# Optimization experiments

Hardware: AMD Instinct MI355X
Metric: run time of the kernel (lower is better)

## Reference

```python
import jax, jax.numpy as jnp
import numpy as np

D_MODEL = 1024
NUM_HEADS = 16
D_K = D_MODEL // NUM_HEADS
B, S = 4, 2048


def setup_inputs() -> dict:
    key = jax.random.key(0)
    ks = jax.random.split(key, 12)
    scale = 1.0 / np.sqrt(D_MODEL)
    inp = {
        "q": jax.random.normal(ks[0], (B, S, D_MODEL), dtype=jnp.float32),
        "k": jax.random.normal(ks[1], (B, S, D_MODEL), dtype=jnp.float32),
        "v": jax.random.normal(ks[2], (B, S, D_MODEL), dtype=jnp.float32),
        "mask": jnp.ones((B, 1, 1, S), dtype=jnp.int32),
        "Wq": jax.random.normal(ks[3], (D_MODEL, D_MODEL), dtype=jnp.float32) * scale,
        "bq": jnp.zeros((D_MODEL,), dtype=jnp.float32),
        "Wk": jax.random.normal(ks[4], (D_MODEL, D_MODEL), dtype=jnp.float32) * scale,
        "bk": jnp.zeros((D_MODEL,), dtype=jnp.float32),
        "Wv": jax.random.normal(ks[5], (D_MODEL, D_MODEL), dtype=jnp.float32) * scale,
        "bv": jnp.zeros((D_MODEL,), dtype=jnp.float32),
        "Wo": jax.random.normal(ks[6], (D_MODEL, D_MODEL), dtype=jnp.float32) * scale,
        "bo": jnp.zeros((D_MODEL,), dtype=jnp.float32),
    }
    return inp


def reference(q, k, v, mask, Wq, bq, Wk, bk, Wv, bv, Wo, bo):
    b, s, d = q.shape
    # QKV projections (torch Linear: x @ W.T + b; here weights stored as (d,d) used as x @ W + b)
    query = (q @ Wq + bq).reshape(b, s, NUM_HEADS, D_K).transpose(0, 2, 1, 3)  # (b,h,s,dk)
    key_ = (k @ Wk + bk).reshape(b, s, NUM_HEADS, D_K).transpose(0, 2, 1, 3)
    value = (v @ Wv + bv).reshape(b, s, NUM_HEADS, D_K).transpose(0, 2, 1, 3)
    # full score matrix (b,h,s,s), scaled by sqrt(d_k)
    scores = jnp.einsum("bhqd,bhkd->bhqk", query, key_) / jnp.sqrt(jnp.float32(D_K))
    scores = jnp.where(mask == 0, jnp.float32(-jnp.inf), scores)
    attn = jax.nn.softmax(scores, axis=-1)
    # dropout p=0.0 (eval) -> identity
    out = jnp.einsum("bhqk,bhkd->bhqd", attn, value)  # (b,h,s,dk)
    out = out.transpose(0, 2, 1, 3).reshape(b, s, NUM_HEADS * D_K)
    return out @ Wo + bo
```

## Files before the change

### kernel.cpp

```cpp
#include <hip/hip_runtime.h>

typedef __attribute__((ext_vector_type(8)))  short  short8;
typedef __attribute__((ext_vector_type(4)))  short  short4v;
typedef __attribute__((ext_vector_type(4)))  float  f32x4;
typedef __attribute__((ext_vector_type(16))) float  f32x16;
typedef __attribute__((ext_vector_type(8)))  __bf16 bf8_t;
typedef __attribute__((ext_vector_type(4)))  __bf16 bf4_t;
typedef __attribute__((ext_vector_type(2)))  __bf16 bf2_t;
typedef __attribute__((ext_vector_type(4)))  unsigned uint4v;

#define DMODEL 1024
#define SEQ    2048
#define NB     4
#define NH     16
#define MTOT   (NB * SEQ)
#define DM2    ((size_t)DMODEL * DMODEL)
#define SCALE_LOG2E 0.18033688011112042f
#define CSTRIDE 512
#define TSPAN   (8 * CSTRIDE)

static __device__ __forceinline__ ushort f2bf(float f) {
  union { float f; unsigned u; } v; v.f = f;
  unsigned r = v.u + 0x7fffu + ((v.u >> 16) & 1u);
  return (ushort)(r >> 16);
}

static __device__ __forceinline__ float fexp2(float x) {
#if __has_builtin(__builtin_amdgcn_exp2f)
  return __builtin_amdgcn_exp2f(x);
#else
  return __expf(x * 0.6931471805599453f);
#endif
}

static __device__ __forceinline__ f32x4 mfma32(short8 a, short8 b, f32x4 c) {
  return __builtin_amdgcn_mfma_f32_16x16x32_bf16(
      __builtin_bit_cast(bf8_t, a), __builtin_bit_cast(bf8_t, b), c, 0, 0, 0);
}

static __device__ __forceinline__ f32x16 mfma3232(short8 a, short8 b, f32x16 c) {
  return __builtin_amdgcn_mfma_f32_32x32x16_bf16(
      __builtin_bit_cast(bf8_t, a), __builtin_bit_cast(bf8_t, b), c, 0, 0, 0);
}

static __device__ __forceinline__ unsigned pk2(float a, float b) {
  bf2_t t; t[0] = (__bf16)a; t[1] = (__bf16)b;
  return __builtin_bit_cast(unsigned, t);
}

static __device__ __forceinline__ void plswap(unsigned& a, unsigned& b) {
  asm volatile("v_permlane32_swap_b32 %0, %1" : "+v"(a), "+v"(b));
}

static __device__ __forceinline__ void gl_lds16(const ushort* g, ushort* l) {
  __builtin_amdgcn_global_load_lds(
      (const __attribute__((address_space(1))) unsigned*)(unsigned long long)g,
      (__attribute__((address_space(3))) unsigned*)(unsigned long long)l,
      16, 0, 0);
}

__global__ __launch_bounds__(256) void cvt3_k(
    const float* __restrict__ q, const float* __restrict__ k,
    const float* __restrict__ v, ushort* __restrict__ qb,
    ushort* __restrict__ kb, ushort* __restrict__ vb,
    const int* __restrict__ mask, float* __restrict__ biasf,
    unsigned* __restrict__ flags) {
  const int z = blockIdx.y;
  if (z == 0 && blockIdx.x < 32) {
    const int t = blockIdx.x * 256 + threadIdx.x;
    const int m = mask[t];
    biasf[t] = m ? 0.f : -1e30f;
    const unsigned long long bal = __ballot(m == 0);
    if ((threadIdx.x & 63) == 0)
      flags[blockIdx.x * 4 + (threadIdx.x >> 6)] = (bal != 0ull) ? 1u : 0u;
  }
  const float* src = (z == 0) ? q : (z == 1) ? k : v;
  ushort* dst = (z == 0) ? qb : (z == 1) ? kb : vb;
  const size_t i = ((size_t)blockIdx.x * 256 + threadIdx.x) * 8;
  const float4 a0 = *(const float4*)&src[i];
  const float4 a1 = *(const float4*)&src[i + 4];
  bf8_t c;
  c[0] = (__bf16)a0.x; c[1] = (__bf16)a0.y; c[2] = (__bf16)a0.z; c[3] = (__bf16)a0.w;
  c[4] = (__bf16)a1.x; c[5] = (__bf16)a1.y; c[6] = (__bf16)a1.z; c[7] = (__bf16)a1.w;
  *(short8*)&dst[i] = __builtin_bit_cast(short8, c);
}

__global__ __launch_bounds__(1024) void wtrans_k(
    const float* __restrict__ Wq, const float* __restrict__ Wk,
    const float* __restrict__ Wv, const float* __restrict__ Wo,
    ushort* __restrict__ Wt) {
  __shared__ float tile[32][33];
  const int z = blockIdx.z;
  const float* W = (z == 0) ? Wq : (z == 1) ? Wk : (z == 2) ? Wv : Wo;
  ushort* out = Wt + (size_t)z * DM2;
  const int tx = threadIdx.x, ty = threadIdx.y;
  const int n0 = blockIdx.x * 32, k0 = blockIdx.y * 32;
  tile[ty][tx] = W[(size_t)(k0 + ty) * DMODEL + n0 + tx];
  __syncthreads();
  out[(size_t)(n0 + ty) * DMODEL + k0 + tx] = f2bf(tile[tx][ty]);
}

#define GEMM_BODY(A, Bt, M0v, N0v)                                              \
  __shared__ ushort Asm[128 * 64];                                              \
  __shared__ ushort Bsm[128 * 64];                                              \
  const int tid = threadIdx.x;                                                  \
  const int wid = tid >> 6, lane = tid & 63;                                    \
  const int wr = wid >> 1, wc = wid & 1;                                        \
  const int lr = lane & 15, lg = lane >> 4;                                     \
  const int m0 = (M0v), n0 = (N0v);                                             \
  const int sr8 = lane >> 3, sg = ((lane & 7) ^ sr8) * 8;                       \
  size_t gA[4], gB[4];                                                          \
  ushort *lA[4], *lB[4];                                                        \
  _Pragma("unroll") for (int j = 0; j < 4; j++) {                               \
    const int ch = wid * 4 + j;                                                 \
    gA[j] = (size_t)(m0 + ch * 8 + sr8) * DMODEL + sg;                          \
    gB[j] = (size_t)(n0 + ch * 8 + sr8) * DMODEL + sg;                          \
    lA[j] = &Asm[ch * 512];                                                     \
    lB[j] = &Bsm[ch * 512];                                                     \
  }                                                                             \
  f32x4 acc[4][4];                                                              \
  _Pragma("unroll") for (int m = 0; m < 4; m++)                                 \
      _Pragma("unroll") for (int n = 0; n < 4; n++)                             \
          acc[m][n] = (f32x4){0.f, 0.f, 0.f, 0.f};                              \
  _Pragma("unroll") for (int j = 0; j < 4; j++) {                               \
    gl_lds16(&A[gA[j]], lA[j]);                                                 \
    gl_lds16(&Bt[gB[j]], lB[j]);                                                \
  }                                                                             \
  const int soff = (lg ^ (lr & 7)) * 8;                                         \
  for (int ks = 0; ks < DMODEL / 64; ++ks) {                                    \
    __syncthreads();                                                            \
    _Pragma("unroll") for (int kk = 0; kk < 2; kk++) {                          \
      const int sx = soff ^ (kk * 32);                                          \
      short8 af[4], bfr[4];                                                     \
      _Pragma("unroll") for (int m = 0; m < 4; m++) af[m] =                     \
          *(const short8*)&Asm[(wr * 64 + m * 16 + lr) * 64 + sx];              \
      _Pragma("unroll") for (int n = 0; n < 4; n++) bfr[n] =                    \
          *(const short8*)&Bsm[(wc * 64 + n * 16 + lr) * 64 + sx];              \
      _Pragma("unroll") for (int m = 0; m < 4; m++)                             \
          _Pragma("unroll") for (int n = 0; n < 4; n++)                         \
              acc[m][n] = mfma32(af[m], bfr[n], acc[m][n]);                     \
    }                                                                           \
    __syncthreads();                                                            \
    if (ks < DMODEL / 64 - 1) {                                                 \
      const size_t ko = (size_t)(ks + 1) * 64;                                  \
      _Pragma("unroll") for (int j = 0; j < 4; j++) {                           \
        gl_lds16(&A[gA[j] + ko], lA[j]);                                        \
        gl_lds16(&Bt[gB[j] + ko], lB[j]);                                       \
      }                                                                         \
    }                                                                           \
  }

__global__ __launch_bounds__(256) void gemmqkv_k(
    const ushort* __restrict__ qb, const ushort* __restrict__ kb,
    const ushort* __restrict__ vb, const ushort* __restrict__ Wt,
    const float* __restrict__ bq, const float* __restrict__ bk,
    const float* __restrict__ bv, ushort* __restrict__ Qp,
    ushort* __restrict__ Kp, ushort* __restrict__ Vb) {
  const int z = blockIdx.z;
  const int bx = blockIdx.x, by = blockIdx.y;
  const ushort* A  = (z == 0) ? Wt : (z == 1) ? (Wt + DM2) : vb;
  const ushort* Bm = (z == 0) ? qb : (z == 1) ? kb : (Wt + 2 * DM2);
  const int M0 = (z == 2) ? bx * 128 : by * 128;
  const int N0 = (z == 2) ? by * 128 : bx * 128;
  GEMM_BODY(A, Bm, M0, N0)

  if (z == 2) {
    float bv4[4];
#pragma unroll
    for (int n = 0; n < 4; n++) bv4[n] = bv[n0 + wc * 64 + n * 16 + lr];
#pragma unroll
    for (int m = 0; m < 4; m++) {
      const int grb = m0 + wr * 64 + m * 16 + lg * 4;
#pragma unroll
      for (int n = 0; n < 4; n++) {
        const int gc = n0 + wc * 64 + n * 16 + lr;
        const int hh = gc >> 6, dk = gc & 63;
        const int bb = grb >> 11, ss = grb & 2047;
        bf4_t pk;
#pragma unroll
        for (int j = 0; j < 4; j++) pk[j] = (__bf16)(acc[m][n][j] + bv4[n]);
        const int swz = ((dk & 7) * 8) ^ (((dk >> 3) & 3) * 16);
        const size_t addr = (((size_t)bb * NH + hh) * SEQ) * 64 +
                            (size_t)(ss >> 6) * 4096 + dk * 64 +
                            ((ss & 63) ^ swz);
        *(short4v*)&Vb[addr] = __builtin_bit_cast(short4v, pk);
      }
    }
  } else {
    const float* bias = (z == 0) ? bq : bk;
    ushort* out = (z == 0) ? Qp : Kp;
    const float scale = (z == 0) ? SCALE_LOG2E : 1.f;
#pragma unroll
    for (int m = 0; m < 4; m++) {
      const int f0 = m0 + wr * 64 + m * 16 + lg * 4;
      const f32x4 b4 = *(const f32x4*)&bias[f0];
      const int hh = f0 >> 6, dk0 = f0 & 63;
#pragma unroll
      for (int n = 0; n < 4; n++) {
        const int t = n0 + wc * 64 + n * 16 + lr;
        const int b = t >> 11, s = t & 2047;
        bf4_t pk;
#pragma unroll
        for (int j = 0; j < 4; j++)
          pk[j] = (__bf16)((acc[m][n][j] + b4[j]) * scale);
        size_t addr;
        if (z == 0) {
          addr = (((size_t)b * NH + hh) * SEQ + s) * 64 + dk0;
        } else {
          const int swz = ((s & 7) * 8) ^ (((s >> 3) & 3) * 16);
          addr = (((size_t)b * NH + hh) * SEQ) * 64 + (size_t)(s >> 6) * 4096 +
                 (s & 63) * 64 + (dk0 ^ swz);
        }
        *(short4v*)&out[addr] = __builtin_bit_cast(short4v, pk);
      }
    }
  }
}

__global__ __launch_bounds__(256) void gemmo_k(
    const ushort* __restrict__ Ain, const ushort* __restrict__ Btin,
    const float* __restrict__ bias, float* __restrict__ out) {
  GEMM_BODY(Ain, Btin, blockIdx.x * 128, blockIdx.y * 128)
  float bv4[4];
#pragma unroll
  for (int n = 0; n < 4; n++) bv4[n] = bias[n0 + wc * 64 + n * 16 + lr];
#pragma unroll
  for (int m = 0; m < 4; m++) {
    const int grb = m0 + wr * 64 + m * 16 + lg * 4;
#pragma unroll
    for (int n = 0; n < 4; n++) {
      const int gc = n0 + wc * 64 + n * 16 + lr;
#pragma unroll
      for (int j = 0; j < 4; j++)
        out[(size_t)(grb + j) * DMODEL + gc] = acc[m][n][j] + bv4[n];
    }
  }
}

__global__ __launch_bounds__(256) void attn_k(
    const ushort* __restrict__ Qp, const ushort* __restrict__ Kp,
    const ushort* __restrict__ Vt, const float* __restrict__ biasf,
    const unsigned* __restrict__ flags, ushort* __restrict__ ctx) {
  __shared__ ushort smem[4 * TSPAN];
  const int tid = threadIdx.x, w = tid >> 6, lane = tid & 63;
  const int q = lane & 31, hi = lane >> 5;
  const int n = blockIdx.x;
  const int xcd = n & 7, idx = n >> 3;
  const int bh = ((idx >> 4) << 3) | xcd;
  const int qt = idx & 15;
  const int b = bh >> 4, h = bh & 15;
  const int q0w = qt * 128 + w * 32;
  const ushort* Qh = Qp + (size_t)bh * SEQ * 64;
  const ushort* Kh = Kp + (size_t)bh * SEQ * 64;
  const ushort* Vh = Vt + (size_t)bh * SEQ * 64;
  const float* biasb = biasf + b * SEQ;
  const unsigned* flb = flags + b * 32;

  short8 qf[4];
#pragma unroll
  for (int c = 0; c < 4; c++)
    qf[c] = *(const short8*)&Qh[(size_t)(q0w + q) * 64 + c * 16 + hi * 8];

  const int xo = ((q & 7) * 8) ^ (((q >> 3) & 3) * 16);
  const int rbase = q * 64;
  int off[4];
#pragma unroll
  for (int c = 0; c < 4; c++) off[c] = rbase + ((c * 16 + hi * 8) ^ xo);

  const int sl = lane * 8;
  const int c0 = 2 * w, c1 = 2 * w + 1;

  f32x16 o0, o1;
#pragma unroll
  for (int r = 0; r < 16; r++) { o0[r] = 0.f; o1[r] = 0.f; }
  float l_run = 0.f;

  gl_lds16(&Kh[c0 * 512 + sl], &smem[c0 * CSTRIDE]);
  gl_lds16(&Kh[c1 * 512 + sl], &smem[c1 * CSTRIDE]);
  gl_lds16(&Vh[c0 * 512 + sl], &smem[2 * TSPAN + c0 * CSTRIDE]);
  gl_lds16(&Vh[c1 * 512 + sl], &smem[2 * TSPAN + c1 * CSTRIDE]);
  __syncthreads();

  for (int it = 0; it < 32; ++it) {
    const int cur = it & 1;
    if (it < 31) {
      const size_t tb = (size_t)(it + 1) * 4096;
      ushort* kd = &smem[(cur ^ 1) * TSPAN];
      ushort* vd = &smem[2 * TSPAN + (cur ^ 1) * TSPAN];
      gl_lds16(&Kh[tb + c0 * 512 + sl], &kd[c0 * CSTRIDE]);
      gl_lds16(&Kh[tb + c1 * 512 + sl], &kd[c1 * CSTRIDE]);
      gl_lds16(&Vh[tb + c0 * 512 + sl], &vd[c0 * CSTRIDE]);
      gl_lds16(&Vh[tb + c1 * 512 + sl], &vd[c1 * CSTRIDE]);
    }

    const ushort* kl = &smem[cur * TSPAN];
    const ushort* vl = &smem[2 * TSPAN + cur * TSPAN];

    f32x16 s0, s1;
#pragma unroll
    for (int r = 0; r < 16; r++) { s0[r] = 0.f; s1[r] = 0.f; }
#pragma unroll
    for (int c = 0; c < 4; c++)
      s0 = mfma3232(*(const short8*)&kl[off[c]], qf[c], s0);
#pragma unroll
    for (int c = 0; c < 4; c++)
      s1 = mfma3232(*(const short8*)&kl[off[c] + 2048], qf[c], s1);

    float p[32];
    if (flb[it]) {
      const float* bp = biasb + it * 64;
#pragma unroll
      for (int kt = 0; kt < 2; kt++)
#pragma unroll
        for (int g = 0; g < 4; g++) {
          const f32x4 ba = *(const f32x4*)&bp[kt * 32 + g * 8 + hi * 4];
#pragma unroll
          for (int j = 0; j < 4; j++)
            p[kt * 16 + g * 4 + j] =
                fexp2((kt ? s1[g * 4 + j] : s0[g * 4 + j]) + ba[j]);
        }
    } else {
#pragma unroll
      for (int r = 0; r < 16; r++) {
        p[r] = fexp2(s0[r]);
        p[16 + r] = fexp2(s1[r]);
      }
    }

    float a16[16], a8[8], a4[4];
#pragma unroll
    for (int i = 0; i < 16; i++) a16[i] = p[i] + p[16 + i];
#pragma unroll
    for (int i = 0; i < 8; i++) a8[i] = a16[i] + a16[8 + i];
#pragma unroll
    for (int i = 0; i < 4; i++) a4[i] = a8[i] + a8[4 + i];
    float ps = (a4[0] + a4[1]) + (a4[2] + a4[3]);
    ps += __shfl_xor(ps, 32);
    l_run += ps;

    short8 frag[4];
#pragma unroll
    for (int kb = 0; kb < 4; kb++) {
      unsigned X0 = pk2(p[8 * kb + 0], p[8 * kb + 1]);
      unsigned X1 = pk2(p[8 * kb + 2], p[8 * kb + 3]);
      unsigned Y0 = pk2(p[8 * kb + 4], p[8 * kb + 5]);
      unsigned Y1 = pk2(p[8 * kb + 6], p[8 * kb + 7]);
      plswap(X0, Y0);
      plswap(X1, Y1);
      frag[kb] = __builtin_bit_cast(short8, (uint4v){X0, X1, Y0, Y1});
    }

#pragma unroll
    for (int kb = 0; kb < 4; kb++) {
      o0 = mfma3232(*(const short8*)&vl[off[kb]], frag[kb], o0);
      o1 = mfma3232(*(const short8*)&vl[off[kb] + 2048], frag[kb], o1);
    }

    __syncthreads();
  }

  const float inv = 1.f / l_run;
  ushort* ow = &smem[w * 2176];
#pragma unroll
  for (int r = 0; r < 16; r++) {
    const int dk = (r & 3) + 8 * (r >> 2) + 4 * hi;
    ow[q * 68 + dk] = __builtin_bit_cast(ushort, (__bf16)(o0[r] * inv));
    ow[q * 68 + 32 + dk] = __builtin_bit_cast(ushort, (__bf16)(o1[r] * inv));
  }
  __syncthreads();
  const int sr = lane >> 4, dc = (lane & 15) * 4;
#pragma unroll
  for (int i = 0; i < 8; i++) {
    const int qq = i * 4 + sr;
    const short4v vv = *(const short4v*)&ow[qq * 68 + dc];
    *(short4v*)&ctx[((size_t)b * SEQ + q0w + qq) * DMODEL + h * 64 + dc] = vv;
  }
}

extern "C" void kernel_launch(void* const* d_in, const int* in_sizes, int n_in,
                              void* d_out, int out_size, void* d_ws,
                              size_t ws_size, hipStream_t stream) {
  const float* q    = (const float*)d_in[0];
  const float* k    = (const float*)d_in[1];
  const float* v    = (const float*)d_in[2];
  const int*   mask = (const int*)d_in[3];
  const float* Wq   = (const float*)d_in[4];
  const float* bq   = (const float*)d_in[5];
  const float* Wk   = (const float*)d_in[6];
  const float* bk   = (const float*)d_in[7];
  const float* Wv   = (const float*)d_in[8];
  const float* bv   = (const float*)d_in[9];
  const float* Wo   = (const float*)d_in[10];
  const float* bo   = (const float*)d_in[11];

  char* p = (char*)d_ws;
  ushort* Wt = (ushort*)p; p += (size_t)4 * DM2 * 2;
  ushort* Qp = (ushort*)p; p += (size_t)MTOT * DMODEL * 2;
  ushort* Kp = (ushort*)p; p += (size_t)MTOT * DMODEL * 2;
  ushort* Vb = (ushort*)p; p += (size_t)MTOT * DMODEL * 2;
  ushort* qb = (ushort*)p; p += (size_t)MTOT * DMODEL * 2;
  ushort* kb = (ushort*)p; p += (size_t)MTOT * DMODEL * 2;
  ushort* vb = (ushort*)p; p += (size_t)MTOT * DMODEL * 2;
  float*  biasf = (float*)p; p += (size_t)NB * SEQ * 4;
  unsigned* flags = (unsigned*)p;
  ushort* ctx = qb;

  wtrans_k<<<dim3(32, 32, 4), dim3(32, 32), 0, stream>>>(Wq, Wk, Wv, Wo, Wt);
  cvt3_k<<<dim3(MTOT * DMODEL / (256 * 8), 3), 256, 0, stream>>>(
      q, k, v, qb, kb, vb, mask, biasf, flags);

  gemmqkv_k<<<dim3(MTOT / 128, DMODEL / 128, 3), 256, 0, stream>>>(
      qb, kb, vb, Wt, bq, bk, bv, Qp, Kp, Vb);

  attn_k<<<1024, 256, 0, stream>>>(Qp, Kp, Vb, biasf, flags, ctx);

  gemmo_k<<<dim3(MTOT / 128, DMODEL / 128), 256, 0, stream>>>(
      ctx, Wt + (size_t)3 * DM2, bo, (float*)d_out);
}
```

Before: 208.2 us.

## Double-buffer GEMM LDS tiles with half-depth K steps and one barrier

Rewrites the shared GEMM body to use two LDS buffers of 128x32 bf16 tiles instead of one 128x64 tile. The next K slice is prefetched into the alternate buffer while MFMAs run on the current one, so each iteration needs one barrier instead of two. The aim is to hide global-to-LDS load latency behind compute. In exchange there are twice as many loop iterations with a smaller K step. The XOR swizzle is narrowed to four 16-byte chunks per row, which may raise LDS bank conflicts.

```diff
diff --git a/kernel.cpp b/kernel.cpp
--- a/kernel.cpp
+++ b/kernel.cpp
@@ -100,54 +100,55 @@
   out[(size_t)(n0 + ty) * DMODEL + k0 + tx] = f2bf(tile[tx][ty]);
 }
 
-#define GEMM_BODY(A, Bt, M0v, N0v)                                              \
-  __shared__ ushort Asm[128 * 64];                                              \
-  __shared__ ushort Bsm[128 * 64];                                              \
-  const int tid = threadIdx.x;                                                  \
-  const int wid = tid >> 6, lane = tid & 63;                                    \
-  const int wr = wid >> 1, wc = wid & 1;                                        \
-  const int lr = lane & 15, lg = lane >> 4;                                     \
-  const int m0 = (M0v), n0 = (N0v);                                             \
-  const int sr8 = lane >> 3, sg = ((lane & 7) ^ sr8) * 8;                       \
-  size_t gA[4], gB[4];                                                          \
-  ushort *lA[4], *lB[4];                                                        \
-  _Pragma("unroll") for (int j = 0; j < 4; j++) {                               \
-    const int ch = wid * 4 + j;                                                 \
-    gA[j] = (size_t)(m0 + ch * 8 + sr8) * DMODEL + sg;                          \
-    gB[j] = (size_t)(n0 + ch * 8 + sr8) * DMODEL + sg;                          \
-    lA[j] = &Asm[ch * 512];                                                     \
-    lB[j] = &Bsm[ch * 512];                                                     \
-  }                                                                             \
-  f32x4 acc[4][4];                                                              \
-  _Pragma("unroll") for (int m = 0; m < 4; m++)                                 \
-      _Pragma("unroll") for (int n = 0; n < 4; n++)                             \
-          acc[m][n] = (f32x4){0.f, 0.f, 0.f, 0.f};                              \
-  _Pragma("unroll") for (int j = 0; j < 4; j++) {                               \
-    gl_lds16(&A[gA[j]], lA[j]);                                                 \
-    gl_lds16(&Bt[gB[j]], lB[j]);                                                \
-  }                                                                             \
-  const int soff = (lg ^ (lr & 7)) * 8;                                         \
-  for (int ks = 0; ks < DMODEL / 64; ++ks) {                                    \
-    __syncthreads();                                                            \
-    _Pragma("unroll") for (int kk = 0; kk < 2; kk++) {                          \
-      const int sx = soff ^ (kk * 32);                                          \
-      short8 af[4], bfr[4];                                                     \
-      _Pragma("unroll") for (int m = 0; m < 4; m++) af[m] =                     \
-          *(const short8*)&Asm[(wr * 64 + m * 16 + lr) * 64 + sx];              \
-      _Pragma("unroll") for (int n = 0; n < 4; n++) bfr[n] =                    \
-          *(const short8*)&Bsm[(wc * 64 + n * 16 + lr) * 64 + sx];              \
-      _Pragma("unroll") for (int m = 0; m < 4; m++)                             \
-          _Pragma("unroll") for (int n = 0; n < 4; n++)                         \
-              acc[m][n] = mfma32(af[m], bfr[n], acc[m][n]);                     \
-    }                                                                           \
-    __syncthreads();                                                            \
-    if (ks < DMODEL / 64 - 1) {                                                 \
-      const size_t ko = (size_t)(ks + 1) * 64;                                  \
-      _Pragma("unroll") for (int j = 0; j < 4; j++) {                           \
-        gl_lds16(&A[gA[j] + ko], lA[j]);                                        \
-        gl_lds16(&Bt[gB[j] + ko], lB[j]);                                       \
-      }                                                                         \
-    }                                                                           \
+#define GEMM_BODY(A, Bt, M0v, N0v)                                             \
+  __shared__ ushort Asm[2][128 * 32];                                          \
+  __shared__ ushort Bsm[2][128 * 32];                                          \
+  const int tid = threadIdx.x;                                                 \
+  const int wid = tid >> 6, lane = tid & 63;                                   \
+  const int wr = wid >> 1, wc = wid & 1;                                       \
+  const int lr = lane & 15, lg = lane >> 4;                                    \
+  const int m0 = (M0v), n0 = (N0v);                                            \
+  const int srow = lane >> 2;                                                  \
+  const int sgr = ((lane & 3) ^ (srow & 3)) * 8;                               \
+  size_t gA[2], gB[2];                                                         \
+  int lco[2];                                                                  \
+  _Pragma("unroll") for (int j = 0; j < 2; j++) {                              \
+    const int ch = wid * 2 + j;                                                \
+    gA[j] = (size_t)(m0 + ch * 16 + srow) * DMODEL + sgr;                      \
+    gB[j] = (size_t)(n0 + ch * 16 + srow) * DMODEL + sgr;                      \
+    lco[j] = ch * 512;                                                         \
+  }                                                                            \
+  f32x4 acc[4][4];                                                             \
+  _Pragma("unroll") for (int m = 0; m < 4; m++)                                \
+      _Pragma("unroll") for (int n = 0; n < 4; n++)                            \
+          acc[m][n] = (f32x4){0.f, 0.f, 0.f, 0.f};                             \
+  _Pragma("unroll") for (int j = 0; j < 2; j++) {                              \
+    gl_lds16(&A[gA[j]], &Asm[0][lco[j]]);                                      \
+    gl_lds16(&Bt[gB[j]], &Bsm[0][lco[j]]);                                     \
+  }                                                                            \
+  __syncthreads();                                                             \
+  const int sx = (lg ^ (lr & 3)) * 8;                                          \
+  int cur = 0;                                                                 \
+  for (int ks = 0; ks < DMODEL / 32; ++ks) {                                   \
+    if (ks < DMODEL / 32 - 1) {                                                \
+      const size_t ko = (size_t)(ks + 1) * 32;                                 \
+      _Pragma("unroll") for (int j = 0; j < 2; j++) {                          \
+        gl_lds16(&A[gA[j] + ko], &Asm[cur ^ 1][lco[j]]);                       \
+        gl_lds16(&Bt[gB[j] + ko], &Bsm[cur ^ 1][lco[j]]);                      \
+      }                                                                        \
+    }                                                                          \
+    const ushort* As = Asm[cur];                                               \
+    const ushort* Bs = Bsm[cur];                                               \
+    short8 af[4], bfr[4];                                                      \
+    _Pragma("unroll") for (int m = 0; m < 4; m++) af[m] =                      \
+        *(const short8*)&As[(wr * 64 + m * 16 + lr) * 32 + sx];                \
+    _Pragma("unroll") for (int n = 0; n < 4; n++) bfr[n] =                     \
+        *(const short8*)&Bs[(wc * 64 + n * 16 + lr) * 32 + sx];                \
+    _Pragma("unroll") for (int m = 0; m < 4; m++)                              \
+        _Pragma("unroll") for (int n = 0; n < 4; n++)                          \
+            acc[m][n] = mfma32(af[m], bfr[n], acc[m][n]);                      \
+    __syncthreads();                                                           \
+    cur ^= 1;                                                                  \
   }
 
 __global__ __launch_bounds__(256) void gemmqkv_k(
```

After: 221.1 us. 1.06x slower.
